# Kernel tuning notes

Measured on AMD Instinct MI355X. Metric: run time of the kernel, lower is better.

## Reference

```python
import jax, jax.numpy as jnp
import numpy as np

N = 50000
E = 1600000
INDIM, HIDIM, OUTDIM = 256, 128, 64


def setup_inputs() -> dict:
    key = jax.random.key(0)
    ks = jax.random.split(key, 4)
    x = jax.random.normal(ks[0], (N, INDIM), dtype=jnp.float32)
    edge_index = jax.random.randint(ks[1], (2, E), 0, N, dtype=jnp.int32)
    W1 = jax.random.normal(ks[2], (INDIM, HIDIM), dtype=jnp.float32) / np.float32(np.sqrt(INDIM))
    b1 = jnp.zeros((HIDIM,), dtype=jnp.float32)
    W2 = jax.random.normal(ks[3], (HIDIM, OUTDIM), dtype=jnp.float32) / np.float32(np.sqrt(HIDIM))
    b2 = jnp.zeros((OUTDIM,), dtype=jnp.float32)
    return {"x": x, "edge_index": edge_index, "W1": W1, "b1": b1, "W2": W2, "b2": b2}


def _gcn_conv(x, row, col, norm, W, b):
    # PyG GCNConv: transform first, then normalized scatter-add aggregation, then bias
    h = x @ W                              # [N, out]
    msg = h[row] * norm[:, None]           # gather source features, scale by edge norm
    out = jax.ops.segment_sum(msg, col, num_segments=x.shape[0])  # scatter-add to dst
    return out + b


def reference(x, edge_index, W1, b1, W2, b2):
    n = x.shape[0]
    # add self loops (PyG default add_self_loops=True)
    loops = jnp.arange(n, dtype=edge_index.dtype)
    row = jnp.concatenate([edge_index[0], loops])  # source nodes
    col = jnp.concatenate([edge_index[1], loops])  # destination nodes
    # symmetric normalization: deg^{-1/2}[row] * deg^{-1/2}[col], deg over dst incl. self loops
    deg = jax.ops.segment_sum(jnp.ones_like(col, dtype=x.dtype), col, num_segments=n)
    dinv = jnp.where(deg > 0, jax.lax.rsqrt(jnp.maximum(deg, 1.0)), 0.0)
    norm = dinv[row] * dinv[col]
    h = jax.nn.relu(_gcn_conv(x, row, col, norm, W1, b1))
    return _gcn_conv(h, row, col, norm, W2, b2)
```

## Files before the change

### kernel.cpp

```cpp
#include <hip/hip_runtime.h>

#define NN 50000
#define NE 1600000
#define INDIM 256
#define HIDIM 128
#define OUTDIM 64

#define NRANGE 64
#define RSPAN 800
#define ACAP 32768
#define NBBLK 1563

typedef unsigned int uint;
typedef unsigned long long ull;
typedef unsigned short ushort;
typedef __attribute__((ext_vector_type(8))) short bf16x8;
typedef __attribute__((ext_vector_type(4))) float f32x4;

__device__ __forceinline__ ushort f2bf(float f) {
    uint u = __float_as_uint(f);
    uint r = (u + 0x7FFFu + ((u >> 16) & 1u)) >> 16;
    return (ushort)r;
}
__device__ __forceinline__ uint pk2(float a, float b) {
    return (uint)f2bf(a) | ((uint)f2bf(b) << 16);
}
__device__ __forceinline__ float bf_lo(uint u) { return __uint_as_float(u << 16); }
__device__ __forceinline__ float bf_hi(uint u) { return __uint_as_float(u & 0xFFFF0000u); }


__global__ void k_wt(const float* __restrict__ W1, const float* __restrict__ W2,
                     ushort* __restrict__ W1T, ushort* __restrict__ W2T) {
    int idx = blockIdx.x * 256 + threadIdx.x;
    if (idx < INDIM * HIDIM) {
        int k = idx / HIDIM, nn = idx % HIDIM;
        W1T[nn * INDIM + k] = f2bf(W1[idx]);
    } else {
        int j = idx - INDIM * HIDIM;
        if (j < HIDIM * OUTDIM) {
            int k = j / OUTDIM, nn = j % OUTDIM;
            W2T[nn * HIDIM + k] = f2bf(W2[j]);
        }
    }
}


__global__ void k_bcnt(const int* __restrict__ col, int* __restrict__ bcnt) {
    __shared__ int bins[NRANGE];
    int tid = threadIdx.x;
    if (tid < NRANGE) bins[tid] = 0;
    __syncthreads();
    int base = blockIdx.x * 1024 + tid;
#pragma unroll
    for (int k = 0; k < 4; k++) {
        int i = base + k * 256;
        if (i < NE) atomicAdd(&bins[col[i] / RSPAN], 1);
    }
    __syncthreads();
    if (tid < NRANGE) bcnt[tid * NBBLK + blockIdx.x] = bins[tid];
}


__global__ void k_bscan(const int* __restrict__ bcnt, int* __restrict__ bbase,
                        int* __restrict__ rcur) {
    __shared__ int wsum[16];
    __shared__ int woff[16];
    int r = blockIdx.x;
    const int* src = bcnt + r * NBBLK;
    int* dst = bbase + r * NBBLK;
    int tid = threadIdx.x, lane = tid & 63, wid = tid >> 6;
    int seg = tid * 2;
    int l0 = (seg < NBBLK) ? src[seg] : 0;
    int l1 = (seg + 1 < NBBLK) ? src[seg + 1] : 0;
    int sum = l0 + l1;
    int incl = sum;
#pragma unroll
    for (int off = 1; off < 64; off <<= 1) {
        int t = __shfl_up(incl, off);
        if (lane >= off) incl += t;
    }
    if (lane == 63) wsum[wid] = incl;
    __syncthreads();
    if (wid == 0 && lane < 16) {
        int wv = wsum[lane];
        int wincl = wv;
#pragma unroll
        for (int off = 1; off < 16; off <<= 1) {
            int t = __shfl_up(wincl, off);
            if (lane >= off) wincl += t;
        }
        woff[lane] = wincl - wv;
    }
    __syncthreads();
    int run = incl - sum + woff[wid];
    if (seg < NBBLK) dst[seg] = run;
    if (seg + 1 < NBBLK) dst[seg + 1] = run + l0;
    if (tid == 1023) rcur[r] = run + sum;
}


__global__ void k_bscat(const int* __restrict__ row, const int* __restrict__ col,
                        const int* __restrict__ bbase, uint* __restrict__ staged) {
    __shared__ int cur[NRANGE];
    int tid = threadIdx.x;
    if (tid < NRANGE) cur[tid] = bbase[tid * NBBLK + blockIdx.x];
    __syncthreads();
    int base = blockIdx.x * 1024 + tid;
#pragma unroll
    for (int k = 0; k < 4; k++) {
        int i = base + k * 256;
        if (i < NE) {
            int d = col[i], s = row[i];
            int r = d / RSPAN;
            int off = atomicAdd(&cur[r], 1);
            staged[(size_t)r * ACAP + off] = ((uint)s << 10) | (uint)(d - r * RSPAN);
        }
    }
}


__global__ void k_sort(const uint* __restrict__ staged, const int* __restrict__ rcur,
                       int* __restrict__ row_ptr, float* __restrict__ dinv,
                       ushort* __restrict__ ssrc) {
    __shared__ int bins[RSPAN];
    __shared__ int wsum[16];
    __shared__ int woff[16];
    int r = blockIdx.x;
    int tid = threadIdx.x, lane = tid & 63, wid = tid >> 6;
    int lo = r * RSPAN;
    int count = rcur[r];
    int base = 0;
    for (int rr = 0; rr < r; rr++) base += rcur[rr];
    const uint* st = staged + (size_t)r * ACAP;

    if (tid < RSPAN) bins[tid] = 0;
    __syncthreads();

    for (int i = tid; i < count; i += 1024)
        atomicAdd(&bins[st[i] & 1023u], 1);
    __syncthreads();

    int v = (tid < RSPAN) ? bins[tid] : 0;
    int incl = v;
#pragma unroll
    for (int off = 1; off < 64; off <<= 1) {
        int t = __shfl_up(incl, off);
        if (lane >= off) incl += t;
    }
    if (lane == 63) wsum[wid] = incl;
    __syncthreads();
    if (wid == 0 && lane < 16) {
        int wv = wsum[lane];
        int wincl = wv;
#pragma unroll
        for (int off = 1; off < 16; off <<= 1) {
            int t = __shfl_up(wincl, off);
            if (lane >= off) wincl += t;
        }
        woff[lane] = wincl - wv;
    }
    __syncthreads();
    int excl = incl - v + woff[wid];
    int idx = lo + tid;
    if (tid < RSPAN && idx <= NN) {
        if (idx < NN) {
            row_ptr[idx] = base + excl;
            dinv[idx] = rsqrtf((float)(v + 1));
        } else {
            row_ptr[NN] = base + excl;
        }
    }
    __syncthreads();
    if (tid < RSPAN) bins[tid] = base + excl;
    __syncthreads();

    for (int i = tid; i < count; i += 1024) {
        uint rec = st[i];
        int pos = atomicAdd(&bins[rec & 1023u], 1);
        ssrc[pos] = (ushort)(rec >> 10);
    }
}


__global__ void k_gemm1(const float* __restrict__ A, const ushort* __restrict__ W1T,
                        const float* __restrict__ dinv, ushort* __restrict__ g1s, int n) {
    __shared__ ushort As[64 * 40];
    __shared__ ushort Bs[128 * 40];
    int tid = threadIdx.x;
    int w = tid >> 6, lane = tid & 63;
    int ln = lane & 15, quad = lane >> 4;
    int row0 = blockIdx.x * 64;
    int n0 = w * 32;

    f32x4 acc[4][2];
#pragma unroll
    for (int m = 0; m < 4; m++)
#pragma unroll
        for (int t = 0; t < 2; t++) acc[m][t] = (f32x4){0.f, 0.f, 0.f, 0.f};

    int ar = tid >> 2;
    int ac = (tid & 3) * 8;

    for (int k0 = 0; k0 < INDIM; k0 += 32) {
        {
            int gr = row0 + ar;
            uint4 u = make_uint4(0, 0, 0, 0);
            if (gr < n) {
                const float* p = A + (size_t)gr * INDIM + k0 + ac;
                float4 v0 = *(const float4*)p;
                float4 v1 = *(const float4*)(p + 4);
                u.x = pk2(v0.x, v0.y); u.y = pk2(v0.z, v0.w);
                u.z = pk2(v1.x, v1.y); u.w = pk2(v1.z, v1.w);
            }
            *(uint4*)(As + ar * 40 + ac) = u;
        }
#pragma unroll
        for (int it = 0; it < 2; it++) {
            int idx = tid + it * 256;
            int bn = idx >> 2, bc = (idx & 3) * 8;
            uint4 u = *(const uint4*)(W1T + (size_t)bn * INDIM + k0 + bc);
            *(uint4*)(Bs + bn * 40 + bc) = u;
        }
        __syncthreads();

        bf16x8 af[4], bf[2];
#pragma unroll
        for (int m = 0; m < 4; m++)
            af[m] = *(const bf16x8*)(As + (m * 16 + ln) * 40 + quad * 8);
#pragma unroll
        for (int t = 0; t < 2; t++)
            bf[t] = *(const bf16x8*)(Bs + (n0 + t * 16 + ln) * 40 + quad * 8);
#pragma unroll
        for (int m = 0; m < 4; m++)
#pragma unroll
            for (int t = 0; t < 2; t++)
                acc[m][t] = __builtin_amdgcn_mfma_f32_16x16x32_bf16(af[m], bf[t], acc[m][t], 0, 0, 0);
        __syncthreads();
    }

#pragma unroll
    for (int m = 0; m < 4; m++) {
#pragma unroll
        for (int r = 0; r < 4; r++) {
            int gr = row0 + m * 16 + quad * 4 + r;
            if (gr < n) {
                float dv = dinv[gr];
#pragma unroll
                for (int t = 0; t < 2; t++) {
                    int cj = t * 16 + ln;
                    g1s[((size_t)w * NN + gr) * 32 + cj] = f2bf(acc[m][t][r] * dv);
                }
            }
        }
    }
}


__global__ void k_agg1(const ushort* __restrict__ g1s, const float* __restrict__ dinv,
                       const int* __restrict__ row_ptr, const ushort* __restrict__ ssrc,
                       const float* __restrict__ b1, ushort* __restrict__ hrb) {
    int slice = blockIdx.x & 3;
    int dbase = (blockIdx.x >> 2) * 32;
    int wid = threadIdx.x >> 6, lane = threadIdx.x & 63;
    int grp = lane >> 3, fl = lane & 7;
    int d = dbase + wid * 8 + grp;
    if (d >= NN) return;
    const ushort* gs = g1s + (size_t)slice * NN * 32 + fl * 4;
    float a0 = 0.f, a1 = 0.f, a2 = 0.f, a3 = 0.f;
    int e0 = row_ptr[d], e1 = row_ptr[d + 1];
    int e = e0;
    for (; e + 1 < e1; e += 2) {
        int s0 = ssrc[e], s1 = ssrc[e + 1];
        uint2 u = *(const uint2*)(gs + (size_t)s0 * 32);
        uint2 v = *(const uint2*)(gs + (size_t)s1 * 32);
        a0 += bf_lo(u.x); a1 += bf_hi(u.x); a2 += bf_lo(u.y); a3 += bf_hi(u.y);
        a0 += bf_lo(v.x); a1 += bf_hi(v.x); a2 += bf_lo(v.y); a3 += bf_hi(v.y);
    }
    if (e < e1) {
        int s0 = ssrc[e];
        uint2 u = *(const uint2*)(gs + (size_t)s0 * 32);
        a0 += bf_lo(u.x); a1 += bf_hi(u.x); a2 += bf_lo(u.y); a3 += bf_hi(u.y);
    }
    uint2 ud = *(const uint2*)(gs + (size_t)d * 32);
    a0 += bf_lo(ud.x); a1 += bf_hi(ud.x); a2 += bf_lo(ud.y); a3 += bf_hi(ud.y);
    float dv = dinv[d];
    float4 bb = *(const float4*)(b1 + slice * 32 + fl * 4);
    ushort4 o;
    o.x = f2bf(fmaxf(a0 * dv + bb.x, 0.f));
    o.y = f2bf(fmaxf(a1 * dv + bb.y, 0.f));
    o.z = f2bf(fmaxf(a2 * dv + bb.z, 0.f));
    o.w = f2bf(fmaxf(a3 * dv + bb.w, 0.f));
    *(ushort4*)(hrb + ((size_t)slice * NN + d) * 32 + fl * 4) = o;
}


__global__ void k_gemm2(const ushort* __restrict__ hrb, const ushort* __restrict__ W2T,
                        const float* __restrict__ dinv, ushort* __restrict__ g2s, int n) {
    __shared__ ushort As[64 * 40];
    __shared__ ushort Bs[64 * 40];
    int tid = threadIdx.x;
    int w = tid >> 6, lane = tid & 63;
    int ln = lane & 15, quad = lane >> 4;
    int row0 = blockIdx.x * 64;
    int n0 = w * 16;

    f32x4 acc[4];
#pragma unroll
    for (int m = 0; m < 4; m++) acc[m] = (f32x4){0.f, 0.f, 0.f, 0.f};

    int ar = tid >> 2;
    int ac = (tid & 3) * 8;

    for (int k0 = 0; k0 < HIDIM; k0 += 32) {
        int hs = k0 >> 5;
        {
            int gr = row0 + ar;
            uint4 u = make_uint4(0, 0, 0, 0);
            if (gr < n) u = *(const uint4*)(hrb + ((size_t)hs * NN + gr) * 32 + ac);
            *(uint4*)(As + ar * 40 + ac) = u;
        }
        {
            int bn = tid >> 2, bc = (tid & 3) * 8;
            uint4 u = *(const uint4*)(W2T + (size_t)bn * HIDIM + k0 + bc);
            *(uint4*)(Bs + bn * 40 + bc) = u;
        }
        __syncthreads();

        bf16x8 bf = *(const bf16x8*)(Bs + (n0 + ln) * 40 + quad * 8);
#pragma unroll
        for (int m = 0; m < 4; m++) {
            bf16x8 af = *(const bf16x8*)(As + (m * 16 + ln) * 40 + quad * 8);
            acc[m] = __builtin_amdgcn_mfma_f32_16x16x32_bf16(af, bf, acc[m], 0, 0, 0);
        }
        __syncthreads();
    }

    int col = n0 + ln;
    int s2 = col >> 5, cj = col & 31;
#pragma unroll
    for (int m = 0; m < 4; m++) {
#pragma unroll
        for (int r = 0; r < 4; r++) {
            int gr = row0 + m * 16 + quad * 4 + r;
            if (gr < n) {
                g2s[((size_t)s2 * NN + gr) * 32 + cj] = f2bf(acc[m][r] * dinv[gr]);
            }
        }
    }
}


__global__ void k_agg2(const ushort* __restrict__ g2s, const float* __restrict__ dinv,
                       const int* __restrict__ row_ptr, const ushort* __restrict__ ssrc,
                       const float* __restrict__ b2, float* __restrict__ out) {
    int slice = blockIdx.x & 1;
    int dbase = (blockIdx.x >> 1) * 32;
    int wid = threadIdx.x >> 6, lane = threadIdx.x & 63;
    int grp = lane >> 3, fl = lane & 7;
    int d = dbase + wid * 8 + grp;
    if (d >= NN) return;
    const ushort* gs = g2s + (size_t)slice * NN * 32 + fl * 4;
    float a0 = 0.f, a1 = 0.f, a2 = 0.f, a3 = 0.f;
    int e0 = row_ptr[d], e1 = row_ptr[d + 1];
    int e = e0;
    for (; e + 1 < e1; e += 2) {
        int s0 = ssrc[e], s1 = ssrc[e + 1];
        uint2 u = *(const uint2*)(gs + (size_t)s0 * 32);
        uint2 v = *(const uint2*)(gs + (size_t)s1 * 32);
        a0 += bf_lo(u.x); a1 += bf_hi(u.x); a2 += bf_lo(u.y); a3 += bf_hi(u.y);
        a0 += bf_lo(v.x); a1 += bf_hi(v.x); a2 += bf_lo(v.y); a3 += bf_hi(v.y);
    }
    if (e < e1) {
        int s0 = ssrc[e];
        uint2 u = *(const uint2*)(gs + (size_t)s0 * 32);
        a0 += bf_lo(u.x); a1 += bf_hi(u.x); a2 += bf_lo(u.y); a3 += bf_hi(u.y);
    }
    uint2 ud = *(const uint2*)(gs + (size_t)d * 32);
    a0 += bf_lo(ud.x); a1 += bf_hi(ud.x); a2 += bf_lo(ud.y); a3 += bf_hi(ud.y);
    float dv = dinv[d];
    float4 bb = *(const float4*)(b2 + slice * 32 + fl * 4);
    float4 r;
    r.x = a0 * dv + bb.x;
    r.y = a1 * dv + bb.y;
    r.z = a2 * dv + bb.z;
    r.w = a3 * dv + bb.w;
    *(float4*)(out + (size_t)d * OUTDIM + slice * 32 + fl * 4) = r;
}


extern "C" void kernel_launch(void* const* d_in, const int* in_sizes, int n_in,
                              void* d_out, int out_size, void* d_ws, size_t ws_size,
                              hipStream_t stream) {
    const float* x   = (const float*)d_in[0];
    const int*   ei  = (const int*)d_in[1];
    const float* W1  = (const float*)d_in[2];
    const float* b1  = (const float*)d_in[3];
    const float* W2  = (const float*)d_in[4];
    const float* b2  = (const float*)d_in[5];
    float* out = (float*)d_out;

    const int* row = ei;
    const int* col = ei + NE;

    size_t off = 0;
    auto alloc = [&](size_t bytes) {
        void* p = (char*)d_ws + off;
        off += (bytes + 255) & ~(size_t)255;
        return p;
    };
    float*  dinv     = (float*) alloc((size_t)NN * 4);
    int*    row_ptr  = (int*)   alloc((size_t)(NN + 1) * 4);
    int*    rcur     = (int*)   alloc(NRANGE * 4);
    int*    bcnt     = (int*)   alloc((size_t)NRANGE * NBBLK * 4);
    int*    bbase    = (int*)   alloc((size_t)NRANGE * NBBLK * 4);
    uint*   staged   = (uint*)  alloc((size_t)NRANGE * ACAP * 4);
    ushort* ssrc     = (ushort*)alloc((size_t)NE * 2);
    ushort* W1T      = (ushort*)alloc((size_t)INDIM * HIDIM * 2);
    ushort* W2T      = (ushort*)alloc((size_t)HIDIM * OUTDIM * 2);
    ushort* g1s      = (ushort*)alloc((size_t)NN * HIDIM * 2);
    ushort* hrb      = (ushort*)alloc((size_t)NN * HIDIM * 2);
    ushort* g2s      = (ushort*)alloc((size_t)NN * OUTDIM * 2);

    const int nb32 = (NN + 31) / 32;
    const int nb64 = (NN + 63) / 64;

    k_wt<<<(INDIM * HIDIM + HIDIM * OUTDIM + 255) / 256, 256, 0, stream>>>(W1, W2, W1T, W2T);

    k_bcnt<<<NBBLK, 256, 0, stream>>>(col, bcnt);
    k_bscan<<<NRANGE, 1024, 0, stream>>>(bcnt, bbase, rcur);
    k_bscat<<<NBBLK, 256, 0, stream>>>(row, col, bbase, staged);

    k_sort<<<NRANGE, 1024, 0, stream>>>(staged, rcur, row_ptr, dinv, ssrc);

    k_gemm1<<<nb64, 256, 0, stream>>>(x, W1T, dinv, g1s, NN);
    k_agg1<<<nb32 * 4, 256, 0, stream>>>(g1s, dinv, row_ptr, ssrc, b1, hrb);
    k_gemm2<<<nb64, 256, 0, stream>>>(hrb, W2T, dinv, g2s, NN);
    k_agg2<<<nb32 * 2, 256, 0, stream>>>(g2s, dinv, row_ptr, ssrc, b2, out);
}
```

Before: 254.7 us.

## Widen aggregation slices to 64 features and software-pipeline neighbor gathers

Changes the intermediate feature layout from 32-wide slices to 64-wide slices, so each aggregation lane gathers 16 bytes (8 bf16) per neighbor instead of 8. This halves the number of aggregation blocks and the repeated index and row_ptr reads. The edge loop is rewritten with a 4-wide, two-stage software prefetch of source indices and features to hide gather latency. The GEMM epilogues and the GEMM2 A-loads are adjusted to match the new layout. In exchange there is more register pressure, and clamped redundant loads are issued on short adjacency lists.

```diff
diff --git a/kernel.cpp b/kernel.cpp
--- a/kernel.cpp
+++ b/kernel.cpp
@@ -27,6 +27,13 @@
 }
 __device__ __forceinline__ float bf_lo(uint u) { return __uint_as_float(u << 16); }
 __device__ __forceinline__ float bf_hi(uint u) { return __uint_as_float(u & 0xFFFF0000u); }
+
+#define ACC8(u) do { \
+    a0 += bf_lo((u).x); a1 += bf_hi((u).x); \
+    a2 += bf_lo((u).y); a3 += bf_hi((u).y); \
+    a4 += bf_lo((u).z); a5 += bf_hi((u).z); \
+    a6 += bf_lo((u).w); a7 += bf_hi((u).w); \
+} while (0)
 
 
 __global__ void k_wt(const float* __restrict__ W1, const float* __restrict__ W2,
@@ -238,6 +245,8 @@
         __syncthreads();
     }
 
+    int slice = w >> 1;
+    int fbase = (w & 1) * 32;
 #pragma unroll
     for (int m = 0; m < 4; m++) {
 #pragma unroll
@@ -248,7 +257,7 @@
 #pragma unroll
                 for (int t = 0; t < 2; t++) {
                     int cj = t * 16 + ln;
-                    g1s[((size_t)w * NN + gr) * 32 + cj] = f2bf(acc[m][t][r] * dv);
+                    g1s[((size_t)slice * NN + gr) * 64 + fbase + cj] = f2bf(acc[m][t][r] * dv);
                 }
             }
         }
@@ -259,38 +268,60 @@
 __global__ void k_agg1(const ushort* __restrict__ g1s, const float* __restrict__ dinv,
                        const int* __restrict__ row_ptr, const ushort* __restrict__ ssrc,
                        const float* __restrict__ b1, ushort* __restrict__ hrb) {
-    int slice = blockIdx.x & 3;
-    int dbase = (blockIdx.x >> 2) * 32;
+    int slice = blockIdx.x & 1;
+    int dbase = (blockIdx.x >> 1) * 32;
     int wid = threadIdx.x >> 6, lane = threadIdx.x & 63;
     int grp = lane >> 3, fl = lane & 7;
     int d = dbase + wid * 8 + grp;
     if (d >= NN) return;
-    const ushort* gs = g1s + (size_t)slice * NN * 32 + fl * 4;
+    const ushort* gs = g1s + (size_t)slice * NN * 64 + fl * 8;
     float a0 = 0.f, a1 = 0.f, a2 = 0.f, a3 = 0.f;
+    float a4 = 0.f, a5 = 0.f, a6 = 0.f, a7 = 0.f;
     int e0 = row_ptr[d], e1 = row_ptr[d + 1];
-    int e = e0;
-    for (; e + 1 < e1; e += 2) {
-        int s0 = ssrc[e], s1 = ssrc[e + 1];
-        uint2 u = *(const uint2*)(gs + (size_t)s0 * 32);
-        uint2 v = *(const uint2*)(gs + (size_t)s1 * 32);
-        a0 += bf_lo(u.x); a1 += bf_hi(u.x); a2 += bf_lo(u.y); a3 += bf_hi(u.y);
-        a0 += bf_lo(v.x); a1 += bf_hi(v.x); a2 += bf_lo(v.y); a3 += bf_hi(v.y);
-    }
-    if (e < e1) {
-        int s0 = ssrc[e];
-        uint2 u = *(const uint2*)(gs + (size_t)s0 * 32);
-        a0 += bf_lo(u.x); a1 += bf_hi(u.x); a2 += bf_lo(u.y); a3 += bf_hi(u.y);
-    }
-    uint2 ud = *(const uint2*)(gs + (size_t)d * 32);
-    a0 += bf_lo(ud.x); a1 += bf_hi(ud.x); a2 += bf_lo(ud.y); a3 += bf_hi(ud.y);
+    if (e1 > e0) {
+        int last = e1 - 1;
+        int sB0 = ssrc[min(e0 + 0, last)];
+        int sB1 = ssrc[min(e0 + 1, last)];
+        int sB2 = ssrc[min(e0 + 2, last)];
+        int sB3 = ssrc[min(e0 + 3, last)];
+        uint4 uA0 = *(const uint4*)(gs + (size_t)sB0 * 64);
+        uint4 uA1 = *(const uint4*)(gs + (size_t)sB1 * 64);
+        uint4 uA2 = *(const uint4*)(gs + (size_t)sB2 * 64);
+        uint4 uA3 = *(const uint4*)(gs + (size_t)sB3 * 64);
+        sB0 = ssrc[min(e0 + 4, last)];
+        sB1 = ssrc[min(e0 + 5, last)];
+        sB2 = ssrc[min(e0 + 6, last)];
+        sB3 = ssrc[min(e0 + 7, last)];
+        for (int eb = e0; eb < e1; eb += 4) {
+            int p0 = ssrc[min(eb + 8, last)];
+            int p1 = ssrc[min(eb + 9, last)];
+            int p2 = ssrc[min(eb + 10, last)];
+            int p3 = ssrc[min(eb + 11, last)];
+            uint4 v0 = *(const uint4*)(gs + (size_t)sB0 * 64);
+            uint4 v1 = *(const uint4*)(gs + (size_t)sB1 * 64);
+            uint4 v2 = *(const uint4*)(gs + (size_t)sB2 * 64);
+            uint4 v3 = *(const uint4*)(gs + (size_t)sB3 * 64);
+            uint4 z = make_uint4(0u, 0u, 0u, 0u);
+            if (eb + 1 >= e1) uA1 = z;
+            if (eb + 2 >= e1) uA2 = z;
+            if (eb + 3 >= e1) uA3 = z;
+            ACC8(uA0); ACC8(uA1); ACC8(uA2); ACC8(uA3);
+            uA0 = v0; uA1 = v1; uA2 = v2; uA3 = v3;
+            sB0 = p0; sB1 = p1; sB2 = p2; sB3 = p3;
+        }
+    }
+    uint4 ud = *(const uint4*)(gs + (size_t)d * 64);
+    ACC8(ud);
     float dv = dinv[d];
-    float4 bb = *(const float4*)(b1 + slice * 32 + fl * 4);
-    ushort4 o;
-    o.x = f2bf(fmaxf(a0 * dv + bb.x, 0.f));
-    o.y = f2bf(fmaxf(a1 * dv + bb.y, 0.f));
-    o.z = f2bf(fmaxf(a2 * dv + bb.z, 0.f));
-    o.w = f2bf(fmaxf(a3 * dv + bb.w, 0.f));
-    *(ushort4*)(hrb + ((size_t)slice * NN + d) * 32 + fl * 4) = o;
+    const float* bp = b1 + slice * 64 + fl * 8;
+    float4 bb0 = *(const float4*)bp;
+    float4 bb1 = *(const float4*)(bp + 4);
+    uint4 o;
+    o.x = pk2(fmaxf(a0 * dv + bb0.x, 0.f), fmaxf(a1 * dv + bb0.y, 0.f));
+    o.y = pk2(fmaxf(a2 * dv + bb0.z, 0.f), fmaxf(a3 * dv + bb0.w, 0.f));
+    o.z = pk2(fmaxf(a4 * dv + bb1.x, 0.f), fmaxf(a5 * dv + bb1.y, 0.f));
+    o.w = pk2(fmaxf(a6 * dv + bb1.z, 0.f), fmaxf(a7 * dv + bb1.w, 0.f));
+    *(uint4*)(hrb + ((size_t)slice * NN + d) * 64 + fl * 8) = o;
 }
 
 
@@ -312,11 +343,10 @@
     int ac = (tid & 3) * 8;
 
     for (int k0 = 0; k0 < HIDIM; k0 += 32) {
-        int hs = k0 >> 5;
         {
             int gr = row0 + ar;
             uint4 u = make_uint4(0, 0, 0, 0);
-            if (gr < n) u = *(const uint4*)(hrb + ((size_t)hs * NN + gr) * 32 + ac);
+            if (gr < n) u = *(const uint4*)(hrb + ((size_t)(k0 >> 6) * NN + gr) * 64 + (k0 & 63) + ac);
             *(uint4*)(As + ar * 40 + ac) = u;
         }
         {
@@ -336,14 +366,13 @@
     }
 
     int col = n0 + ln;
-    int s2 = col >> 5, cj = col & 31;
 #pragma unroll
     for (int m = 0; m < 4; m++) {
 #pragma unroll
         for (int r = 0; r < 4; r++) {
             int gr = row0 + m * 16 + quad * 4 + r;
             if (gr < n) {
-                g2s[((size_t)s2 * NN + gr) * 32 + cj] = f2bf(acc[m][r] * dinv[gr]);
+                g2s[(size_t)gr * 64 + col] = f2bf(acc[m][r] * dinv[gr]);
             }
         }
     }
@@ -353,38 +382,65 @@
 __global__ void k_agg2(const ushort* __restrict__ g2s, const float* __restrict__ dinv,
                        const int* __restrict__ row_ptr, const ushort* __restrict__ ssrc,
                        const float* __restrict__ b2, float* __restrict__ out) {
-    int slice = blockIdx.x & 1;
-    int dbase = (blockIdx.x >> 1) * 32;
+    int dbase = blockIdx.x * 32;
     int wid = threadIdx.x >> 6, lane = threadIdx.x & 63;
     int grp = lane >> 3, fl = lane & 7;
     int d = dbase + wid * 8 + grp;
     if (d >= NN) return;
-    const ushort* gs = g2s + (size_t)slice * NN * 32 + fl * 4;
+    const ushort* gs = g2s + fl * 8;
     float a0 = 0.f, a1 = 0.f, a2 = 0.f, a3 = 0.f;
+    float a4 = 0.f, a5 = 0.f, a6 = 0.f, a7 = 0.f;
     int e0 = row_ptr[d], e1 = row_ptr[d + 1];
-    int e = e0;
-    for (; e + 1 < e1; e += 2) {
-        int s0 = ssrc[e], s1 = ssrc[e + 1];
-        uint2 u = *(const uint2*)(gs + (size_t)s0 * 32);
-        uint2 v = *(const uint2*)(gs + (size_t)s1 * 32);
-        a0 += bf_lo(u.x); a1 += bf_hi(u.x); a2 += bf_lo(u.y); a3 += bf_hi(u.y);
-        a0 += bf_lo(v.x); a1 += bf_hi(v.x); a2 += bf_lo(v.y); a3 += bf_hi(v.y);
-    }
-    if (e < e1) {
-        int s0 = ssrc[e];
-        uint2 u = *(const uint2*)(gs + (size_t)s0 * 32);
-        a0 += bf_lo(u.x); a1 += bf_hi(u.x); a2 += bf_lo(u.y); a3 += bf_hi(u.y);
-    }
-    uint2 ud = *(const uint2*)(gs + (size_t)d * 32);
-    a0 += bf_lo(ud.x); a1 += bf_hi(ud.x); a2 += bf_lo(ud.y); a3 += bf_hi(ud.y);
+    if (e1 > e0) {
+        int last = e1 - 1;
+        int sB0 = ssrc[min(e0 + 0, last)];
+        int sB1 = ssrc[min(e0 + 1, last)];
+        int sB2 = ssrc[min(e0 + 2, last)];
+        int sB3 = ssrc[min(e0 + 3, last)];
+        uint4 uA0 = *(const uint4*)(gs + (size_t)sB0 * 64);
+        uint4 uA1 = *(const uint4*)(gs + (size_t)sB1 * 64);
+        uint4 uA2 = *(const uint4*)(gs + (size_t)sB2 * 64);
+        uint4 uA3 = *(const uint4*)(gs + (size_t)sB3 * 64);
+        sB0 = ssrc[min(e0 + 4, last)];
+        sB1 = ssrc[min(e0 + 5, last)];
+        sB2 = ssrc[min(e0 + 6, last)];
+        sB3 = ssrc[min(e0 + 7, last)];
+        for (int eb = e0; eb < e1; eb += 4) {
+            int p0 = ssrc[min(eb + 8, last)];
+            int p1 = ssrc[min(eb + 9, last)];
+            int p2 = ssrc[min(eb + 10, last)];
+            int p3 = ssrc[min(eb + 11, last)];
+            uint4 v0 = *(const uint4*)(gs + (size_t)sB0 * 64);
+            uint4 v1 = *(const uint4*)(gs + (size_t)sB1 * 64);
+            uint4 v2 = *(const uint4*)(gs + (size_t)sB2 * 64);
+            uint4 v3 = *(const uint4*)(gs + (size_t)sB3 * 64);
+            uint4 z = make_uint4(0u, 0u, 0u, 0u);
+            if (eb + 1 >= e1) uA1 = z;
+            if (eb + 2 >= e1) uA2 = z;
+            if (eb + 3 >= e1) uA3 = z;
+            ACC8(uA0); ACC8(uA1); ACC8(uA2); ACC8(uA3);
+            uA0 = v0; uA1 = v1; uA2 = v2; uA3 = v3;
+            sB0 = p0; sB1 = p1; sB2 = p2; sB3 = p3;
+        }
+    }
+    uint4 ud = *(const uint4*)(gs + (size_t)d * 64);
+    ACC8(ud);
     float dv = dinv[d];
-    float4 bb = *(const float4*)(b2 + slice * 32 + fl * 4);
-    float4 r;
-    r.x = a0 * dv + bb.x;
-    r.y = a1 * dv + bb.y;
-    r.z = a2 * dv + bb.z;
-    r.w = a3 * dv + bb.w;
-    *(float4*)(out + (size_t)d * OUTDIM + slice * 32 + fl * 4) = r;
+    const float* bp = b2 + fl * 8;
+    float4 bb0 = *(const float4*)bp;
+    float4 bb1 = *(const float4*)(bp + 4);
+    float4 r0, r1;
+    r0.x = a0 * dv + bb0.x;
+    r0.y = a1 * dv + bb0.y;
+    r0.z = a2 * dv + bb0.z;
+    r0.w = a3 * dv + bb0.w;
+    r1.x = a4 * dv + bb1.x;
+    r1.y = a5 * dv + bb1.y;
+    r1.z = a6 * dv + bb1.z;
+    r1.w = a7 * dv + bb1.w;
+    float* op = out + (size_t)d * OUTDIM + fl * 8;
+    *(float4*)op = r0;
+    *(float4*)(op + 4) = r1;
 }
 
 
@@ -433,7 +489,7 @@
     k_sort<<<NRANGE, 1024, 0, stream>>>(staged, rcur, row_ptr, dinv, ssrc);
 
     k_gemm1<<<nb64, 256, 0, stream>>>(x, W1T, dinv, g1s, NN);
-    k_agg1<<<nb32 * 4, 256, 0, stream>>>(g1s, dinv, row_ptr, ssrc, b1, hrb);
+    k_agg1<<<nb32 * 2, 256, 0, stream>>>(g1s, dinv, row_ptr, ssrc, b1, hrb);
     k_gemm2<<<nb64, 256, 0, stream>>>(hrb, W2T, dinv, g2s, NN);
-    k_agg2<<<nb32 * 2, 256, 0, stream>>>(g2s, dinv, row_ptr, ssrc, b2, out);
-}
+    k_agg2<<<nb32, 256, 0, stream>>>(g2s, dinv, row_ptr, ssrc, b2, out);
+}
```

After: 222.0 us. 1.15x faster.
